# Performance work log

Measured on AMD Instinct MI355X. Metric: run time of the kernel, lower is better.

The kernel has to match this reference:

```python
import jax, jax.numpy as jnp
import numpy as np

N_SRC, N_MID, N_OUT = 100000, 20000, 5000
E1, E2 = 20000, 20000
IN, H, EF = 64, 64, 32


def setup_inputs() -> dict:
    key = jax.random.key(0)
    ks = jax.random.split(key, 12)
    s = 1.0 / np.sqrt(EF)
    return {
        "in_feat": jax.random.normal(ks[0], (N_SRC, IN), jnp.float32),
        "edge_feats": jax.random.normal(ks[1], (E1, EF), jnp.float32),
        "edge_feats1": jax.random.normal(ks[2], (E2, EF), jnp.float32),
        "W1": jax.random.uniform(ks[3], (EF, IN * H), jnp.float32, -s, s),
        "b1": jax.random.uniform(ks[4], (IN * H,), jnp.float32, -s, s),
        "W2": jax.random.uniform(ks[5], (EF, H * H), jnp.float32, -s, s),
        "b2": jax.random.uniform(ks[6], (H * H,), jnp.float32, -s, s),
        "src1": jax.random.randint(ks[7], (E1,), 0, N_SRC, jnp.int32),
        "dst1": jax.random.randint(ks[8], (E1,), 0, N_MID, jnp.int32),
        "src2": jax.random.randint(ks[9], (E2,), 0, N_MID, jnp.int32),
        "dst2": jax.random.randint(ks[10], (E2,), 0, N_OUT, jnp.int32),
    }


def nnconv_mean(h, efeat, W, b, src, dst, n_dst, d_in, d_out):
    # per-edge weight matrix from edge MLP: [E, d_in, d_out]
    We = (efeat @ W + b).reshape(-1, d_in, d_out)
    # gather src feats and apply per-edge matmul: [E, d_out]
    msg = jnp.einsum("ei,eio->eo", h[src], We)
    # scatter-mean into dst nodes (empty dst -> 0, matching DGL mean)
    sums = jax.ops.segment_sum(msg, dst, num_segments=n_dst)
    cnt = jax.ops.segment_sum(jnp.ones((dst.shape[0],), msg.dtype), dst,
                              num_segments=n_dst)
    return sums / jnp.maximum(cnt, 1.0)[:, None]


def reference(in_feat, edge_feats, edge_feats1, W1, b1, W2, b2,
              src1, dst1, src2, dst2):
    h = nnconv_mean(in_feat, edge_feats, W1, b1, src1, dst1, N_MID, IN, H)
    h = jax.nn.relu(h)
    h = nnconv_mean(h, edge_feats1, W2, b2, src2, dst2, N_OUT, H, H)
    return h
```

## Files before the change

kernel.cpp:

```cpp
#include <hip/hip_runtime.h>
#include <hip/hip_bf16.h>

#define N_SRC 100000
#define N_MID 20000
#define N_OUT 5000
#define E_1   20000
#define E_2   20000
#define NCHUNK 33
#define NSPLIT 4
#define NBLK   313
#define EPAD   (NBLK*64)
#define MAXDEG 32

typedef float f32x4 __attribute__((ext_vector_type(4)));
typedef short s16x8 __attribute__((ext_vector_type(8)));

__device__ __forceinline__ void load_lds16(const void* g, void* l) {
    __builtin_amdgcn_global_load_lds(
        (const __attribute__((address_space(1))) unsigned int*)g,
        (__attribute__((address_space(3))) unsigned int*)l, 16, 0, 0);
}

__device__ __forceinline__ s16x8 pack_bf16x8(float4 x, float4 y, float s) {
    union { s16x8 v; __hip_bfloat162 h[4]; } u;
    u.h[0] = __float22bfloat162_rn(make_float2(s * x.x, s * x.y));
    u.h[1] = __float22bfloat162_rn(make_float2(s * x.z, s * x.w));
    u.h[2] = __float22bfloat162_rn(make_float2(s * y.x, s * y.y));
    u.h[3] = __float22bfloat162_rn(make_float2(s * y.z, s * y.w));
    return u.v;
}

__device__ __forceinline__ unsigned short f2bf_rne(float f) {
    unsigned u = __float_as_uint(f);
    return (unsigned short)((u + 0x7FFFu + ((u >> 16) & 1u)) >> 16);
}

__global__ void prep_kernel(const float* __restrict__ W1, const float* __restrict__ b1,
                            const float* __restrict__ W2, const float* __restrict__ b2,
                            uint4* __restrict__ Wt1, uint4* __restrict__ Wt2)
{
    int gid = blockIdx.x * 256 + threadIdx.x;
    if (gid >= 2 * NCHUNK * 512) return;
    int layer = gid / (NCHUNK * 512);
    int r     = gid % (NCHUNK * 512);
    int c  = r / 512;
    int u  = r % 512;
    int k8 = u / 64;
    int n  = u % 64;
    const float* W = layer ? W2 : W1;
    const float* b = layer ? b2 : b1;
    const float* s = (c < 32) ? (W + (size_t)c * 4096) : b;
    union { uint4 v; unsigned short us[8]; } pk;
    #pragma unroll
    for (int j = 0; j < 8; ++j)
        pk.us[j] = f2bf_rne(s[(k8 * 8 + j) * 64 + n]);
    uint4* Wt = layer ? Wt2 : Wt1;
    Wt[(size_t)c * 512 + n * 8 + (k8 ^ (n & 7))] = pk.v;
}

__global__ void count_slot_kernel(const int* __restrict__ dst1, const int* __restrict__ dst2,
                                  int* __restrict__ cur1, int* __restrict__ slots1,
                                  int* __restrict__ cur2, int* __restrict__ slots2)
{
    int i = blockIdx.x * blockDim.x + threadIdx.x;
    if (i < E_1) {
        int d = dst1[i];
        int p = atomicAdd(&cur1[d], 1);
        if (p < MAXDEG) slots1[(size_t)d * MAXDEG + p] = i;
    } else if (i < E_1 + E_2) {
        int e = i - E_1;
        int d = dst2[e];
        int p = atomicAdd(&cur2[d], 1);
        if (p < MAXDEG) slots2[(size_t)d * MAXDEG + p] = e;
    }
}

__global__ __launch_bounds__(256) void nnconv_mfma(
    const float* __restrict__ h,
    const float* __restrict__ efeat,
    const uint4* __restrict__ Wt,
    const int*  __restrict__ src,
    int E,
    float* __restrict__ msg)
{
    __shared__ float efs[64][9];
    __shared__ uint4 wbuf[2][512];

    const int t  = threadIdx.x;
    const int w  = t >> 6;
    const int l  = t & 63;
    const int m15 = l & 15;
    const int q   = l >> 4;
    const int ebase = blockIdx.x * 64;
    const int split = blockIdx.y;
    const int c_lo = (split == 0) ? 0 : (split * 8 + 1);
    const int c_hi = split * 8 + 9;
    const int nc   = c_hi - c_lo;

    for (int idx = t; idx < 64 * nc; idx += 256) {
        int e = idx / nc, j = idx - e * nc;
        int eg = ebase + e, f = c_lo + j;
        float v = 0.0f;
        if (eg < E) v = (f < 32) ? efeat[eg * 32 + f] : 1.0f;
        efs[e][j] = v;
    }

    {
        const uint4* g = Wt + (size_t)c_lo * 512;
        load_lds16(g + t,       &wbuf[0][t]);
        load_lds16(g + 256 + t, &wbuf[0][256 + t]);
    }

    const int e_a = ebase + w * 16 + m15;
    const int row = (e_a < E) ? src[e_a] : 0;
    const float* hp = h + (size_t)row * 64 + q * 8;
    const float4 ha0 = *(const float4*)(hp);
    const float4 ha1 = *(const float4*)(hp + 4);
    const float4 hb0 = *(const float4*)(hp + 32);
    const float4 hb1 = *(const float4*)(hp + 36);

    f32x4 acc[4] = {};
    const int nx = m15 & 7;

    int cur = 0;
    for (int c = c_lo; c < c_hi; ++c) {
        __syncthreads();
        if (c + 1 < c_hi) {
            const uint4* g = Wt + (size_t)(c + 1) * 512;
            load_lds16(g + t,       &wbuf[cur ^ 1][t]);
            load_lds16(g + 256 + t, &wbuf[cur ^ 1][256 + t]);
        }
        const float ef = efs[w * 16 + m15][c - c_lo];
        const s16x8 a0 = pack_bf16x8(ha0, ha1, ef);
        const s16x8 a1 = pack_bf16x8(hb0, hb1, ef);
        const uint4* wb = wbuf[cur];
        #pragma unroll
        for (int c16 = 0; c16 < 4; ++c16) {
            const int n = c16 * 16 + m15;
            const s16x8 b0 = *(const s16x8*)&wb[n * 8 + ((q)     ^ nx)];
            const s16x8 b1 = *(const s16x8*)&wb[n * 8 + ((4 + q) ^ nx)];
            acc[c16] = __builtin_amdgcn_mfma_f32_16x16x32_bf16(a0, b0, acc[c16], 0, 0, 0);
            acc[c16] = __builtin_amdgcn_mfma_f32_16x16x32_bf16(a1, b1, acc[c16], 0, 0, 0);
        }
        cur ^= 1;
    }

    float* mp = msg + (size_t)split * EPAD * 64;
    #pragma unroll
    for (int r = 0; r < 4; ++r) {
        float* rp = mp + (size_t)(ebase + w * 16 + q * 4 + r) * 64 + m15;
        #pragma unroll
        for (int c16 = 0; c16 < 4; ++c16)
            rp[c16 * 16] = acc[c16][r];
    }
}

__global__ void gather_mean(const float* __restrict__ msg,
                            const int* __restrict__ slots, const int* __restrict__ cur,
                            int n_dst, int do_relu, float* __restrict__ outp)
{
    int d = blockIdx.x * 4 + (threadIdx.x >> 6);
    int o = threadIdx.x & 63;
    if (d >= n_dst) return;
    int deg = cur[d];
    int dg = min(deg, MAXDEG);
    float s = 0.0f;
    for (int j = 0; j < dg; ++j) {
        int e = slots[(size_t)d * MAXDEG + j];
        const float* mrow = msg + (size_t)e * 64 + o;
        #pragma unroll
        for (int sp = 0; sp < NSPLIT; ++sp)
            s += mrow[(size_t)sp * EPAD * 64];
    }
    s *= 1.0f / fmaxf((float)deg, 1.0f);
    if (do_relu) s = fmaxf(s, 0.0f);
    outp[(size_t)d * 64 + o] = s;
}

extern "C" void kernel_launch(void* const* d_in, const int* in_sizes, int n_in,
                              void* d_out, int out_size, void* d_ws, size_t ws_size,
                              hipStream_t stream)
{
    const float* in_feat = (const float*)d_in[0];
    const float* ef1     = (const float*)d_in[1];
    const float* ef2     = (const float*)d_in[2];
    const float* W1      = (const float*)d_in[3];
    const float* b1      = (const float*)d_in[4];
    const float* W2      = (const float*)d_in[5];
    const float* b2      = (const float*)d_in[6];
    const int*   src1    = (const int*)d_in[7];
    const int*   dst1    = (const int*)d_in[8];
    const int*   src2    = (const int*)d_in[9];
    const int*   dst2    = (const int*)d_in[10];

    float* h_mid  = (float*)d_ws;
    int*   cur1   = (int*)(h_mid + (size_t)N_MID * 64);
    int*   cur2   = cur1 + N_MID;
    int*   slots1 = cur2 + N_OUT;
    int*   slots2 = slots1 + (size_t)N_MID * MAXDEG;
    uint4* Wt1    = (uint4*)(slots2 + (size_t)N_OUT * MAXDEG);
    uint4* Wt2    = Wt1 + (size_t)NCHUNK * 512;
    float* msg    = (float*)(Wt2 + (size_t)NCHUNK * 512);
    float* out    = (float*)d_out;

    hipMemsetAsync(cur1, 0, (size_t)(N_MID + N_OUT) * sizeof(int), stream);

    prep_kernel<<<(2 * NCHUNK * 512 + 255) / 256, 256, 0, stream>>>(W1, b1, W2, b2, Wt1, Wt2);
    count_slot_kernel<<<(E_1 + E_2 + 255) / 256, 256, 0, stream>>>(dst1, dst2,
                                                                   cur1, slots1, cur2, slots2);

    dim3 grid(NBLK, NSPLIT);
    nnconv_mfma<<<grid, 256, 0, stream>>>(in_feat, ef1, Wt1, src1, E_1, msg);
    gather_mean<<<(N_MID + 3) / 4, 256, 0, stream>>>(msg, slots1, cur1, N_MID, 1, h_mid);

    nnconv_mfma<<<grid, 256, 0, stream>>>(h_mid, ef2, Wt2, src2, E_2, msg);
    gather_mean<<<(N_OUT + 3) / 4, 256, 0, stream>>>(msg, slots2, cur2, N_OUT, 0, out);
}
```

Baseline: 146.0 us.

## Replace slot-based gather-mean with atomic scatter-add and fold mean/relu into next layer

Drops the per-destination slot lists and gather_mean kernels. The MFMA kernel now atomically adds each message straight into per-destination sums. The mean division and ReLU of layer 1 are applied when layer 2 loads its source rows, and a small finalize kernel divides the output sums by degree. Setup work (weight prep, degree counting, zeroing the accumulators) is merged into one kernel, and the chunk split goes from 4 to 2 to cut the number of atomic adds. This removes the MAXDEG cap and the large message buffer traffic, at the cost of float atomics with nondeterministic summation order and fewer blocks.

After: 146.5 us. No clear change (+0.3%).

```diff
diff --git a/kernel.cpp b/kernel.cpp
--- a/kernel.cpp
+++ b/kernel.cpp
@@ -7,10 +7,8 @@
 #define E_1   20000
 #define E_2   20000
 #define NCHUNK 33
-#define NSPLIT 4
+#define NSPLIT 2
 #define NBLK   313
-#define EPAD   (NBLK*64)
-#define MAXDEG 32
 
 typedef float f32x4 __attribute__((ext_vector_type(4)));
 typedef short s16x8 __attribute__((ext_vector_type(8)));
@@ -35,55 +33,61 @@
     return (unsigned short)((u + 0x7FFFu + ((u >> 16) & 1u)) >> 16);
 }
 
-__global__ void prep_kernel(const float* __restrict__ W1, const float* __restrict__ b1,
-                            const float* __restrict__ W2, const float* __restrict__ b2,
-                            uint4* __restrict__ Wt1, uint4* __restrict__ Wt2)
+__device__ __forceinline__ float4 relu_scale4(float4 v, float s) {
+    return make_float4(fmaxf(v.x * s, 0.0f), fmaxf(v.y * s, 0.0f),
+                       fmaxf(v.z * s, 0.0f), fmaxf(v.w * s, 0.0f));
+}
+
+__global__ void setup_kernel(const float* __restrict__ W1, const float* __restrict__ b1,
+                             const float* __restrict__ W2, const float* __restrict__ b2,
+                             uint4* __restrict__ Wt1, uint4* __restrict__ Wt2,
+                             const int* __restrict__ dst1, const int* __restrict__ dst2,
+                             int* __restrict__ cur1, int* __restrict__ cur2,
+                             float4* __restrict__ zbase)
 {
     int gid = blockIdx.x * 256 + threadIdx.x;
-    if (gid >= 2 * NCHUNK * 512) return;
-    int layer = gid / (NCHUNK * 512);
-    int r     = gid % (NCHUNK * 512);
-    int c  = r / 512;
-    int u  = r % 512;
-    int k8 = u / 64;
-    int n  = u % 64;
-    const float* W = layer ? W2 : W1;
-    const float* b = layer ? b2 : b1;
-    const float* s = (c < 32) ? (W + (size_t)c * 4096) : b;
-    union { uint4 v; unsigned short us[8]; } pk;
-    #pragma unroll
-    for (int j = 0; j < 8; ++j)
-        pk.us[j] = f2bf_rne(s[(k8 * 8 + j) * 64 + n]);
-    uint4* Wt = layer ? Wt2 : Wt1;
-    Wt[(size_t)c * 512 + n * 8 + (k8 ^ (n & 7))] = pk.v;
-}
-
-__global__ void count_slot_kernel(const int* __restrict__ dst1, const int* __restrict__ dst2,
-                                  int* __restrict__ cur1, int* __restrict__ slots1,
-                                  int* __restrict__ cur2, int* __restrict__ slots2)
-{
-    int i = blockIdx.x * blockDim.x + threadIdx.x;
-    if (i < E_1) {
-        int d = dst1[i];
-        int p = atomicAdd(&cur1[d], 1);
-        if (p < MAXDEG) slots1[(size_t)d * MAXDEG + p] = i;
-    } else if (i < E_1 + E_2) {
-        int e = i - E_1;
-        int d = dst2[e];
-        int p = atomicAdd(&cur2[d], 1);
-        if (p < MAXDEG) slots2[(size_t)d * MAXDEG + p] = e;
-    }
-}
-
+
+    if (gid < 2 * NCHUNK * 512) {
+        int layer = gid / (NCHUNK * 512);
+        int r     = gid % (NCHUNK * 512);
+        int c  = r / 512;
+        int u  = r % 512;
+        int k8 = u / 64;
+        int n  = u % 64;
+        const float* W = layer ? W2 : W1;
+        const float* b = layer ? b2 : b1;
+        const float* s = (c < 32) ? (W + (size_t)c * 4096) : b;
+        union { uint4 v; unsigned short us[8]; } pk;
+        #pragma unroll
+        for (int j = 0; j < 8; ++j)
+            pk.us[j] = f2bf_rne(s[(k8 * 8 + j) * 64 + n]);
+        uint4* Wt = layer ? Wt2 : Wt1;
+        Wt[(size_t)c * 512 + n * 8 + (k8 ^ (n & 7))] = pk.v;
+    }
+
+    if (gid < E_1) {
+        atomicAdd(&cur1[dst1[gid]], 1);
+    } else if (gid < E_1 + E_2) {
+        atomicAdd(&cur2[dst2[gid - E_1]], 1);
+    }
+
+    const int ZN4 = (N_MID + N_OUT) * 16;
+    for (int i = gid; i < ZN4; i += gridDim.x * 256)
+        zbase[i] = make_float4(0.0f, 0.0f, 0.0f, 0.0f);
+}
+
+template<int NORM>
 __global__ __launch_bounds__(256) void nnconv_mfma(
     const float* __restrict__ h,
     const float* __restrict__ efeat,
     const uint4* __restrict__ Wt,
     const int*  __restrict__ src,
+    const int*  __restrict__ dstv,
+    const int*  __restrict__ degs,
     int E,
-    float* __restrict__ msg)
-{
-    __shared__ float efs[64][9];
+    float* __restrict__ outacc)
+{
+    __shared__ float efs[64][17];
     __shared__ uint4 wbuf[2][512];
 
     const int t  = threadIdx.x;
@@ -93,8 +97,8 @@
     const int q   = l >> 4;
     const int ebase = blockIdx.x * 64;
     const int split = blockIdx.y;
-    const int c_lo = (split == 0) ? 0 : (split * 8 + 1);
-    const int c_hi = split * 8 + 9;
+    const int c_lo = split ? 17 : 0;
+    const int c_hi = split ? 33 : 17;
     const int nc   = c_hi - c_lo;
 
     for (int idx = t; idx < 64 * nc; idx += 256) {
@@ -111,13 +115,27 @@
         load_lds16(g + 256 + t, &wbuf[0][256 + t]);
     }
 
+    int dv[4];
+    #pragma unroll
+    for (int r = 0; r < 4; ++r) {
+        int e = ebase + w * 16 + q * 4 + r;
+        dv[r] = (e < E) ? dstv[e] : 0;
+    }
+
     const int e_a = ebase + w * 16 + m15;
     const int row = (e_a < E) ? src[e_a] : 0;
     const float* hp = h + (size_t)row * 64 + q * 8;
-    const float4 ha0 = *(const float4*)(hp);
-    const float4 ha1 = *(const float4*)(hp + 4);
-    const float4 hb0 = *(const float4*)(hp + 32);
-    const float4 hb1 = *(const float4*)(hp + 36);
+    float4 ha0 = *(const float4*)(hp);
+    float4 ha1 = *(const float4*)(hp + 4);
+    float4 hb0 = *(const float4*)(hp + 32);
+    float4 hb1 = *(const float4*)(hp + 36);
+    if (NORM) {
+        const float rd = 1.0f / fmaxf((float)degs[row], 1.0f);
+        ha0 = relu_scale4(ha0, rd);
+        ha1 = relu_scale4(ha1, rd);
+        hb0 = relu_scale4(hb0, rd);
+        hb1 = relu_scale4(hb1, rd);
+    }
 
     f32x4 acc[4] = {};
     const int nx = m15 & 7;
@@ -145,36 +163,26 @@
         cur ^= 1;
     }
 
-    float* mp = msg + (size_t)split * EPAD * 64;
     #pragma unroll
     for (int r = 0; r < 4; ++r) {
-        float* rp = mp + (size_t)(ebase + w * 16 + q * 4 + r) * 64 + m15;
+        float* rp = outacc + (size_t)dv[r] * 64 + m15;
         #pragma unroll
         for (int c16 = 0; c16 < 4; ++c16)
-            rp[c16 * 16] = acc[c16][r];
-    }
-}
-
-__global__ void gather_mean(const float* __restrict__ msg,
-                            const int* __restrict__ slots, const int* __restrict__ cur,
-                            int n_dst, int do_relu, float* __restrict__ outp)
-{
-    int d = blockIdx.x * 4 + (threadIdx.x >> 6);
-    int o = threadIdx.x & 63;
-    if (d >= n_dst) return;
-    int deg = cur[d];
-    int dg = min(deg, MAXDEG);
-    float s = 0.0f;
-    for (int j = 0; j < dg; ++j) {
-        int e = slots[(size_t)d * MAXDEG + j];
-        const float* mrow = msg + (size_t)e * 64 + o;
-        #pragma unroll
-        for (int sp = 0; sp < NSPLIT; ++sp)
-            s += mrow[(size_t)sp * EPAD * 64];
-    }
-    s *= 1.0f / fmaxf((float)deg, 1.0f);
-    if (do_relu) s = fmaxf(s, 0.0f);
-    outp[(size_t)d * 64 + o] = s;
+            unsafeAtomicAdd(rp + c16 * 16, acc[c16][r]);
+    }
+}
+
+__global__ void finalize_kernel(const float4* __restrict__ outsum,
+                                const int* __restrict__ cur,
+                                float4* __restrict__ outp)
+{
+    int i = blockIdx.x * 256 + threadIdx.x;
+    if (i >= N_OUT * 16) return;
+    int d = i >> 4;
+    float rd = 1.0f / fmaxf((float)cur[d], 1.0f);
+    float4 v = outsum[i];
+    v.x *= rd; v.y *= rd; v.z *= rd; v.w *= rd;
+    outp[i] = v;
 }
 
 extern "C" void kernel_launch(void* const* d_in, const int* in_sizes, int n_in,
@@ -193,26 +201,24 @@
     const int*   src2    = (const int*)d_in[9];
     const int*   dst2    = (const int*)d_in[10];
 
-    float* h_mid  = (float*)d_ws;
-    int*   cur1   = (int*)(h_mid + (size_t)N_MID * 64);
+    uint4* Wt1    = (uint4*)d_ws;
+    uint4* Wt2    = Wt1 + (size_t)NCHUNK * 512;
+    float* hsum   = (float*)(Wt2 + (size_t)NCHUNK * 512);
+    float* outsum = hsum + (size_t)N_MID * 64;
+    int*   cur1   = (int*)(outsum + (size_t)N_OUT * 64);
     int*   cur2   = cur1 + N_MID;
-    int*   slots1 = cur2 + N_OUT;
-    int*   slots2 = slots1 + (size_t)N_MID * MAXDEG;
-    uint4* Wt1    = (uint4*)(slots2 + (size_t)N_OUT * MAXDEG);
-    uint4* Wt2    = Wt1 + (size_t)NCHUNK * 512;
-    float* msg    = (float*)(Wt2 + (size_t)NCHUNK * 512);
     float* out    = (float*)d_out;
 
     hipMemsetAsync(cur1, 0, (size_t)(N_MID + N_OUT) * sizeof(int), stream);
 
-    prep_kernel<<<(2 * NCHUNK * 512 + 255) / 256, 256, 0, stream>>>(W1, b1, W2, b2, Wt1, Wt2);
-    count_slot_kernel<<<(E_1 + E_2 + 255) / 256, 256, 0, stream>>>(dst1, dst2,
-                                                                   cur1, slots1, cur2, slots2);
+    setup_kernel<<<1024, 256, 0, stream>>>(W1, b1, W2, b2, Wt1, Wt2,
+                                           dst1, dst2, cur1, cur2, (float4*)hsum);
 
     dim3 grid(NBLK, NSPLIT);
-    nnconv_mfma<<<grid, 256, 0, stream>>>(in_feat, ef1, Wt1, src1, E_1, msg);
-    gather_mean<<<(N_MID + 3) / 4, 256, 0, stream>>>(msg, slots1, cur1, N_MID, 1, h_mid);
-
-    nnconv_mfma<<<grid, 256, 0, stream>>>(h_mid, ef2, Wt2, src2, E_2, msg);
-    gather_mean<<<(N_OUT + 3) / 4, 256, 0, stream>>>(msg, slots2, cur2, N_OUT, 0, out);
-}
+    nnconv_mfma<0><<<grid, 256, 0, stream>>>(in_feat, ef1, Wt1, src1, dst1,
+                                             nullptr, E_1, hsum);
+    nnconv_mfma<1><<<grid, 256, 0, stream>>>(hsum, ef2, Wt2, src2, dst2,
+                                             cur1, E_2, outsum);
+    finalize_kernel<<<(N_OUT * 16 + 255) / 256, 256, 0, stream>>>(
+        (const float4*)outsum, cur2, (float4*)out);
+}
```
